# Kernel optimization log

Measured on AMD Instinct MI355X. Metric: run time of the kernel, lower is better.

The kernel has to match this reference:

```python
import jax, jax.numpy as jnp
import numpy as np

H = 6  # num_heads
D = 384  # embedding_dim


def _rot(seg, coord):
    # seg: [BN, H, T, L], coord: [BN, T]; rotate interleaved even/odd pairs
    L = seg.shape[-1]
    pairs = max(L // 2, 1)
    inv_freq = 1.0 / (10000.0 ** (jnp.arange(pairs, dtype=seg.dtype) / pairs))
    ang = coord[..., None] * inv_freq          # [BN, T, pairs]
    cos = jnp.cos(ang)[:, None]                # [BN, 1, T, pairs]
    sin = jnp.sin(ang)[:, None]
    even, odd = seg[..., 0::2], seg[..., 1::2]
    re = even * cos - odd * sin
    ro = even * sin + odd * cos
    return jnp.stack((re, ro), axis=-1).reshape(seg.shape)


def _apply_rope3(t, pos, chunk):
    # t: [BN, H, T, Hd], pos: [BN, T, 3]; three axis chunks, tail untouched
    parts, s = [], 0
    for i in range(3):
        parts.append(_rot(t[..., s:s + chunk], pos[..., i]))
        s += chunk
    parts.append(t[..., s:])
    return jnp.concatenate(parts, axis=-1)


def setup_inputs() -> dict:
    key = jax.random.key(0)
    ks = jax.random.split(key, 10)
    B, N, T = 8, 64, 128
    scale = 1.0 / np.sqrt(D)
    return {
        "padded_batches": jax.random.normal(ks[0], (B, N, T, D), jnp.float32),
        "sum_token": jax.random.normal(ks[1], (B, N, 1, D), jnp.float32),
        "positions_3d": jax.random.uniform(ks[2], (B, N, T, 3), jnp.float32),
        "Wq": jax.random.normal(ks[3], (D, D), jnp.float32) * scale,
        "bq": jax.random.normal(ks[4], (D,), jnp.float32) * scale,
        "Wk": jax.random.normal(ks[5], (D, D), jnp.float32) * scale,
        "bk": jax.random.normal(ks[6], (D,), jnp.float32) * scale,
        "Wv": jax.random.normal(ks[7], (D, D), jnp.float32) * scale,
        "bv": jax.random.normal(ks[8], (D,), jnp.float32) * scale,
        "masks": jax.random.randint(ks[9], (B, N, T), 0, 2, jnp.int32),
    }


def reference(padded_batches, sum_token, positions_3d, Wq, bq, Wk, bk, Wv, bv, masks):
    B, N, T, Dm = padded_batches.shape
    Hd = Dm // H
    chunk = Hd // 6 * 2

    # masked mean-pool summary token (summary_mode='avg')
    w = masks[..., None].astype(padded_batches.dtype)          # [B,N,T,1]
    denom = jnp.clip(w.sum(axis=-2, keepdims=True), 1e-6, None)
    summary = (padded_batches * w).sum(axis=-2, keepdims=True) / denom  # [B,N,1,D]

    q = (padded_batches @ Wq + bq).reshape(B * N, T, H, Hd).transpose(0, 2, 1, 3)  # [BN,H,T,Hd]
    k = (summary @ Wk + bk).reshape(B * N, 1, H, Hd).transpose(0, 2, 1, 3)         # [BN,H,1,Hd]
    v = (summary @ Wv + bv).reshape(B * N, 1, H, Hd).transpose(0, 2, 1, 3)

    # 3-axis RoPE on q (token positions) and k (pooled positions)
    pos_summary = (positions_3d * w).sum(axis=-2, keepdims=True) / denom  # [B,N,1,3]
    pos_q = positions_3d.reshape(B * N, T, 3)
    pos_k = pos_summary.reshape(B * N, 1, 3)
    q = _apply_rope3(q, pos_q, chunk)
    k = _apply_rope3(k, pos_k, chunk)

    # SDPA with T queries vs 1 key
    scores = jnp.einsum('bhtd,bhkd->bhtk', q, k) / np.float32(np.sqrt(Hd))  # [BN,H,T,1]
    mask_add = jnp.where(masks.reshape(B * N, 1, T, 1) == 0,
                         jnp.finfo(jnp.float32).min, 0.0)
    attn_w = jax.nn.softmax(scores + mask_add, axis=-1)
    attn = jnp.einsum('bhtk,bhkd->bhtd', attn_w, v)  # [BN,H,T,Hd]

    out = attn.transpose(0, 2, 1, 3).reshape(B, N, T, Dm) + padded_batches
    return out
```

## Files before the change

### kernel.cpp

```cpp
#include <hip/hip_runtime.h>
#include <hip/hip_bf16.h>


#define DM 384
#define TT 128
#define C4 96
#define BN_TOT 512

__global__ __launch_bounds__(384) void k1_partial_sums(
    const float* __restrict__ padded,
    const int*   __restrict__ masks,
    float*       __restrict__ ws_part)
{
    const int bn   = blockIdx.x >> 1;
    const int half = blockIdx.x & 1;
    const int t = threadIdx.x;
    const int c = t % C4;
    const int r = t / C4;

    __shared__ float  w_sh[64];
    __shared__ float4 part_sh[4][C4];

    if (t < 64) w_sh[t] = (float)masks[bn * TT + half * 64 + t];
    __syncthreads();

    const float4* __restrict__ p4 =
        (const float4*)(padded + (size_t)bn * TT * DM) + half * 64 * C4;

    float4 acc = make_float4(0.f, 0.f, 0.f, 0.f);
    #pragma unroll
    for (int i = 0; i < 16; ++i) {
        const int    tt = r + i * 4;
        const float  w  = w_sh[tt];
        const float4 x  = p4[tt * C4 + c];
        acc.x += x.x * w; acc.y += x.y * w; acc.z += x.z * w; acc.w += x.w * w;
    }
    part_sh[r][c] = acc;
    __syncthreads();

    if (t < C4) {
        const float4 a0 = part_sh[0][t], a1 = part_sh[1][t];
        const float4 a2 = part_sh[2][t], a3 = part_sh[3][t];
        float4 s;
        s.x = a0.x + a1.x + a2.x + a3.x;
        s.y = a0.y + a1.y + a2.y + a3.y;
        s.z = a0.z + a1.z + a2.z + a3.z;
        s.w = a0.w + a1.w + a2.w + a3.w;
        ((float4*)(ws_part + ((size_t)bn * 2 + half) * DM))[t] = s;
    }
}

__global__ __launch_bounds__(384) void k2_matvec(
    const float* __restrict__ ws_part,
    const int*   __restrict__ masks,
    const float* __restrict__ Wv,
    const float* __restrict__ bv,
    float*       __restrict__ ws_v)
{
    const int bn0 = blockIdx.x * 2;
    const int bn1 = bn0 + 1;
    const int t = threadIdx.x;
    const int c = t % C4;
    const int r = t / C4;

    __shared__ float summ0[DM], summ1[DM];
    __shared__ float4 part0[4][C4], part1[4][C4];
    __shared__ float w0_sh[TT], w1_sh[TT];

    if (t < TT) w0_sh[t] = (float)masks[bn0 * TT + t];
    else if (t < 2 * TT) w1_sh[t - TT] = (float)masks[bn1 * TT + (t - TT)];
    __syncthreads();

    if (t < C4) {
        float ws0 = 0.f, ws1 = 0.f;
        #pragma unroll
        for (int i = 0; i < TT; ++i) { ws0 += w0_sh[i]; ws1 += w1_sh[i]; }
        const float id0 = 1.0f / fmaxf(ws0, 1e-6f);
        const float id1 = 1.0f / fmaxf(ws1, 1e-6f);
        const float4 p00 = ((const float4*)(ws_part + (size_t)bn0 * 2 * DM))[t];
        const float4 p01 = ((const float4*)(ws_part + ((size_t)bn0 * 2 + 1) * DM))[t];
        const float4 p10 = ((const float4*)(ws_part + (size_t)bn1 * 2 * DM))[t];
        const float4 p11 = ((const float4*)(ws_part + ((size_t)bn1 * 2 + 1) * DM))[t];
        float4 s0, s1;
        s0.x = (p00.x + p01.x) * id0; s0.y = (p00.y + p01.y) * id0;
        s0.z = (p00.z + p01.z) * id0; s0.w = (p00.w + p01.w) * id0;
        s1.x = (p10.x + p11.x) * id1; s1.y = (p10.y + p11.y) * id1;
        s1.z = (p10.z + p11.z) * id1; s1.w = (p10.w + p11.w) * id1;
        ((float4*)summ0)[t] = s0;
        ((float4*)summ1)[t] = s1;
    }
    __syncthreads();

    float4 a0 = make_float4(0.f, 0.f, 0.f, 0.f);
    float4 a1 = make_float4(0.f, 0.f, 0.f, 0.f);
    const int e0 = r * C4;
    #pragma unroll 8
    for (int i = 0; i < C4; ++i) {
        const int   e  = e0 + i;
        const float s0 = summ0[e];
        const float s1 = summ1[e];
        const float4 wv = *(const float4*)(Wv + (size_t)e * DM + 4 * c);
        a0.x += s0 * wv.x; a0.y += s0 * wv.y; a0.z += s0 * wv.z; a0.w += s0 * wv.w;
        a1.x += s1 * wv.x; a1.y += s1 * wv.y; a1.z += s1 * wv.z; a1.w += s1 * wv.w;
    }
    part0[r][c] = a0;
    part1[r][c] = a1;
    __syncthreads();

    if (t < C4) {
        const float4 b = ((const float4*)bv)[t];
        float4 v0 = b, v1 = b;
        #pragma unroll
        for (int g = 0; g < 4; ++g) {
            const float4 q0 = part0[g][t], q1 = part1[g][t];
            v0.x += q0.x; v0.y += q0.y; v0.z += q0.z; v0.w += q0.w;
            v1.x += q1.x; v1.y += q1.y; v1.z += q1.z; v1.w += q1.w;
        }
        ((float4*)(ws_v + (size_t)bn0 * DM))[t] = v0;
        ((float4*)(ws_v + (size_t)bn1 * DM))[t] = v1;
    }
}

__global__ __launch_bounds__(384) void k3_add(
    const float* __restrict__ padded,
    const float* __restrict__ ws_v,
    float*       __restrict__ out)
{
    const int bn = blockIdx.x >> 2;
    const int q  = blockIdx.x & 3;
    const int t = threadIdx.x;
    const int c = t % C4;
    const int r = t / C4;

    __shared__ float4 v_sh[C4];
    if (t < C4) v_sh[t] = ((const float4*)(ws_v + (size_t)bn * DM))[t];
    __syncthreads();

    const size_t base = (size_t)bn * TT * C4 + (size_t)q * 32 * C4;
    const float4* __restrict__ p4 = (const float4*)padded + base;
    float4*       __restrict__ o4 = (float4*)out + base;

    const float4 v = v_sh[c];
    #pragma unroll
    for (int i = 0; i < 8; ++i) {
        const int tt = r + i * 4;
        float4 x = p4[tt * C4 + c];
        x.x += v.x; x.y += v.y; x.z += v.z; x.w += v.w;
        o4[tt * C4 + c] = x;
    }
}

extern "C" void kernel_launch(void* const* d_in, const int* in_sizes, int n_in,
                              void* d_out, int out_size, void* d_ws, size_t ws_size,
                              hipStream_t stream) {
    const float* padded = (const float*)d_in[0];
    const float* Wv     = (const float*)d_in[7];
    const float* bv     = (const float*)d_in[8];
    const int*   masks  = (const int*)d_in[9];
    float* out = (float*)d_out;

    float* ws_part = (float*)d_ws;
    float* ws_v    = ws_part + (size_t)BN_TOT * 2 * DM;

    k1_partial_sums<<<BN_TOT * 2, 384, 0, stream>>>(padded, masks, ws_part);
    k2_matvec<<<BN_TOT / 2, 384, 0, stream>>>(ws_part, masks, Wv, bv, ws_v);
    k3_add<<<BN_TOT * 4, 384, 0, stream>>>(padded, ws_v, out);
}
```

Baseline: 222.0 us.

## Fuse masked mean, value matvec and residual add into one register-resident kernel

Replaces the three-kernel pipeline with a single kernel per (b,n) that loads the 128x384 tile into registers once. It computes the masked mean, the Wv matvec and the residual add, then writes output from the held registers. This removes the second read of the input, the workspace round trips and two launches. In exchange, each block holds many registers, runs with 768 threads and fewer blocks, and serializes the matvec between the read and write phases.

```diff
diff --git a/kernel.cpp b/kernel.cpp
--- a/kernel.cpp
+++ b/kernel.cpp
@@ -1,152 +1,100 @@
 #include <hip/hip_runtime.h>
-#include <hip/hip_bf16.h>
 
 
 #define DM 384
 #define TT 128
 #define C4 96
 #define BN_TOT 512
+#define NR  8
+#define RPT 16
 
-__global__ __launch_bounds__(384) void k1_partial_sums(
+__global__ __launch_bounds__(768) void fused_mean_matvec_add(
     const float* __restrict__ padded,
     const int*   __restrict__ masks,
-    float*       __restrict__ ws_part)
+    const float* __restrict__ Wv,
+    const float* __restrict__ bv,
+    float*       __restrict__ out)
 {
-    const int bn   = blockIdx.x >> 1;
-    const int half = blockIdx.x & 1;
-    const int t = threadIdx.x;
-    const int c = t % C4;
-    const int r = t / C4;
+    const int bn = blockIdx.x;
+    const int t  = threadIdx.x;
+    const int c  = t % C4;
+    const int r  = t / C4;
 
-    __shared__ float  w_sh[64];
-    __shared__ float4 part_sh[4][C4];
-
-    if (t < 64) w_sh[t] = (float)masks[bn * TT + half * 64 + t];
-    __syncthreads();
+    __shared__ float  w_sh[TT];
+    __shared__ float4 part_sh[NR][C4];
+    __shared__ float  summ[DM];
+    __shared__ float4 v_sh[C4];
 
     const float4* __restrict__ p4 =
-        (const float4*)(padded + (size_t)bn * TT * DM) + half * 64 * C4;
+        (const float4*)padded + (size_t)bn * TT * C4;
+
+    float4 x[RPT];
+    #pragma unroll
+    for (int i = 0; i < RPT; ++i) {
+        x[i] = p4[(r + i * NR) * C4 + c];
+    }
+
+    if (t < TT) w_sh[t] = (float)masks[bn * TT + t];
+    __syncthreads();
 
     float4 acc = make_float4(0.f, 0.f, 0.f, 0.f);
     #pragma unroll
-    for (int i = 0; i < 16; ++i) {
-        const int    tt = r + i * 4;
-        const float  w  = w_sh[tt];
-        const float4 x  = p4[tt * C4 + c];
-        acc.x += x.x * w; acc.y += x.y * w; acc.z += x.z * w; acc.w += x.w * w;
+    for (int i = 0; i < RPT; ++i) {
+        const float w = w_sh[r + i * NR];
+        acc.x += x[i].x * w; acc.y += x[i].y * w;
+        acc.z += x[i].z * w; acc.w += x[i].w * w;
     }
     part_sh[r][c] = acc;
     __syncthreads();
 
     if (t < C4) {
-        const float4 a0 = part_sh[0][t], a1 = part_sh[1][t];
-        const float4 a2 = part_sh[2][t], a3 = part_sh[3][t];
-        float4 s;
-        s.x = a0.x + a1.x + a2.x + a3.x;
-        s.y = a0.y + a1.y + a2.y + a3.y;
-        s.z = a0.z + a1.z + a2.z + a3.z;
-        s.w = a0.w + a1.w + a2.w + a3.w;
-        ((float4*)(ws_part + ((size_t)bn * 2 + half) * DM))[t] = s;
+        float dsum = 0.f;
+        #pragma unroll
+        for (int i = 0; i < TT; ++i) dsum += w_sh[i];
+        const float inv = 1.0f / fmaxf(dsum, 1e-6f);
+
+        float4 s = part_sh[0][t];
+        #pragma unroll
+        for (int g = 1; g < NR; ++g) {
+            const float4 p = part_sh[g][t];
+            s.x += p.x; s.y += p.y; s.z += p.z; s.w += p.w;
+        }
+        s.x *= inv; s.y *= inv; s.z *= inv; s.w *= inv;
+        ((float4*)summ)[t] = s;
     }
-}
+    __syncthreads();
 
-__global__ __launch_bounds__(384) void k2_matvec(
-    const float* __restrict__ ws_part,
-    const int*   __restrict__ masks,
-    const float* __restrict__ Wv,
-    const float* __restrict__ bv,
-    float*       __restrict__ ws_v)
-{
-    const int bn0 = blockIdx.x * 2;
-    const int bn1 = bn0 + 1;
-    const int t = threadIdx.x;
-    const int c = t % C4;
-    const int r = t / C4;
-
-    __shared__ float summ0[DM], summ1[DM];
-    __shared__ float4 part0[4][C4], part1[4][C4];
-    __shared__ float w0_sh[TT], w1_sh[TT];
-
-    if (t < TT) w0_sh[t] = (float)masks[bn0 * TT + t];
-    else if (t < 2 * TT) w1_sh[t - TT] = (float)masks[bn1 * TT + (t - TT)];
+    float4 a = make_float4(0.f, 0.f, 0.f, 0.f);
+    const float4* __restrict__ wv4 = (const float4*)Wv;
+    const int e0 = r * (DM / NR);
+    #pragma unroll 8
+    for (int i = 0; i < DM / NR; ++i) {
+        const int   e = e0 + i;
+        const float s = summ[e];
+        const float4 w = wv4[(size_t)e * C4 + c];
+        a.x += s * w.x; a.y += s * w.y; a.z += s * w.z; a.w += s * w.w;
+    }
+    part_sh[r][c] = a;
     __syncthreads();
 
     if (t < C4) {
-        float ws0 = 0.f, ws1 = 0.f;
+        float4 v = ((const float4*)bv)[t];
         #pragma unroll
-        for (int i = 0; i < TT; ++i) { ws0 += w0_sh[i]; ws1 += w1_sh[i]; }
-        const float id0 = 1.0f / fmaxf(ws0, 1e-6f);
-        const float id1 = 1.0f / fmaxf(ws1, 1e-6f);
-        const float4 p00 = ((const float4*)(ws_part + (size_t)bn0 * 2 * DM))[t];
-        const float4 p01 = ((const float4*)(ws_part + ((size_t)bn0 * 2 + 1) * DM))[t];
-        const float4 p10 = ((const float4*)(ws_part + (size_t)bn1 * 2 * DM))[t];
-        const float4 p11 = ((const float4*)(ws_part + ((size_t)bn1 * 2 + 1) * DM))[t];
-        float4 s0, s1;
-        s0.x = (p00.x + p01.x) * id0; s0.y = (p00.y + p01.y) * id0;
-        s0.z = (p00.z + p01.z) * id0; s0.w = (p00.w + p01.w) * id0;
-        s1.x = (p10.x + p11.x) * id1; s1.y = (p10.y + p11.y) * id1;
-        s1.z = (p10.z + p11.z) * id1; s1.w = (p10.w + p11.w) * id1;
-        ((float4*)summ0)[t] = s0;
-        ((float4*)summ1)[t] = s1;
+        for (int g = 0; g < NR; ++g) {
+            const float4 p = part_sh[g][t];
+            v.x += p.x; v.y += p.y; v.z += p.z; v.w += p.w;
+        }
+        v_sh[t] = v;
     }
     __syncthreads();
 
-    float4 a0 = make_float4(0.f, 0.f, 0.f, 0.f);
-    float4 a1 = make_float4(0.f, 0.f, 0.f, 0.f);
-    const int e0 = r * C4;
-    #pragma unroll 8
-    for (int i = 0; i < C4; ++i) {
-        const int   e  = e0 + i;
-        const float s0 = summ0[e];
-        const float s1 = summ1[e];
-        const float4 wv = *(const float4*)(Wv + (size_t)e * DM + 4 * c);
-        a0.x += s0 * wv.x; a0.y += s0 * wv.y; a0.z += s0 * wv.z; a0.w += s0 * wv.w;
-        a1.x += s1 * wv.x; a1.y += s1 * wv.y; a1.z += s1 * wv.z; a1.w += s1 * wv.w;
-    }
-    part0[r][c] = a0;
-    part1[r][c] = a1;
-    __syncthreads();
-
-    if (t < C4) {
-        const float4 b = ((const float4*)bv)[t];
-        float4 v0 = b, v1 = b;
-        #pragma unroll
-        for (int g = 0; g < 4; ++g) {
-            const float4 q0 = part0[g][t], q1 = part1[g][t];
-            v0.x += q0.x; v0.y += q0.y; v0.z += q0.z; v0.w += q0.w;
-            v1.x += q1.x; v1.y += q1.y; v1.z += q1.z; v1.w += q1.w;
-        }
-        ((float4*)(ws_v + (size_t)bn0 * DM))[t] = v0;
-        ((float4*)(ws_v + (size_t)bn1 * DM))[t] = v1;
-    }
-}
-
-__global__ __launch_bounds__(384) void k3_add(
-    const float* __restrict__ padded,
-    const float* __restrict__ ws_v,
-    float*       __restrict__ out)
-{
-    const int bn = blockIdx.x >> 2;
-    const int q  = blockIdx.x & 3;
-    const int t = threadIdx.x;
-    const int c = t % C4;
-    const int r = t / C4;
-
-    __shared__ float4 v_sh[C4];
-    if (t < C4) v_sh[t] = ((const float4*)(ws_v + (size_t)bn * DM))[t];
-    __syncthreads();
-
-    const size_t base = (size_t)bn * TT * C4 + (size_t)q * 32 * C4;
-    const float4* __restrict__ p4 = (const float4*)padded + base;
-    float4*       __restrict__ o4 = (float4*)out + base;
-
     const float4 v = v_sh[c];
+    float4* __restrict__ o4 = (float4*)out + (size_t)bn * TT * C4;
     #pragma unroll
-    for (int i = 0; i < 8; ++i) {
-        const int tt = r + i * 4;
-        float4 x = p4[tt * C4 + c];
-        x.x += v.x; x.y += v.y; x.z += v.z; x.w += v.w;
-        o4[tt * C4 + c] = x;
+    for (int i = 0; i < RPT; ++i) {
+        float4 y = x[i];
+        y.x += v.x; y.y += v.y; y.z += v.z; y.w += v.w;
+        o4[(r + i * NR) * C4 + c] = y;
     }
 }
 
@@ -159,10 +107,5 @@
     const int*   masks  = (const int*)d_in[9];
     float* out = (float*)d_out;
 
-    float* ws_part = (float*)d_ws;
-    float* ws_v    = ws_part + (size_t)BN_TOT * 2 * DM;
-
-    k1_partial_sums<<<BN_TOT * 2, 384, 0, stream>>>(padded, masks, ws_part);
-    k2_matvec<<<BN_TOT / 2, 384, 0, stream>>>(ws_part, masks, Wv, bv, ws_v);
-    k3_add<<<BN_TOT * 4, 384, 0, stream>>>(padded, ws_v, out);
+    fused_mean_matvec_add<<<BN_TOT, 768, 0, stream>>>(padded, masks, Wv, bv, out);
 }
```

After: 211.8 us. 4.6% less time.
